# Kernel tuning notes

Hardware: AMD Instinct MI355X
Metric: run time of the kernel (lower is better)

The kernel has to match this reference:

```python
import jax, jax.numpy as jnp
import numpy as np

EMBED_DIM = 1024
NUM_HEADS = 16
HEAD_DIM = EMBED_DIM // NUM_HEADS


def setup_inputs() -> dict:
    key = jax.random.key(0)
    ks = jax.random.split(key, 6)
    B, S, D = 4, 2048, EMBED_DIM
    std = 1.0 / np.sqrt(D)
    x = jax.random.normal(ks[0], (B, S, D), dtype=jnp.float32)
    wq = jax.random.normal(ks[1], (D, D), dtype=jnp.float32) * std
    wk = jax.random.normal(ks[2], (D, D), dtype=jnp.float32) * std
    wv = jax.random.normal(ks[3], (D, D), dtype=jnp.float32) * std
    wo = jax.random.normal(ks[4], (D, D), dtype=jnp.float32) * std
    bo = jax.random.normal(ks[5], (D,), dtype=jnp.float32) * 0.01
    return {"x": x, "wq": wq, "wk": wk, "wv": wv, "wo": wo, "bo": bo}


def reference(x, wq, wk, wv, wo, bo):
    B, S, D = x.shape
    H, Hd = NUM_HEADS, HEAD_DIM
    scale = 1.0 / jnp.sqrt(jnp.asarray(Hd, x.dtype))
    # nn.Linear computes x @ W.T; split into heads -> [B, H, S, Hd]
    q = (x @ wq.T).reshape(B, S, H, Hd).transpose(0, 2, 1, 3)
    k = (x @ wk.T).reshape(B, S, H, Hd).transpose(0, 2, 1, 3)
    v = (x @ wv.T).reshape(B, S, H, Hd).transpose(0, 2, 1, 3)
    scores = jnp.einsum("bhqd,bhkd->bhqk", q, k) * scale  # [B,H,S,S]
    attn = jax.nn.softmax(scores, axis=-1)
    ctx = jnp.einsum("bhqk,bhkd->bhqd", attn, v)
    ctx = ctx.transpose(0, 2, 1, 3).reshape(B, S, D)
    return ctx @ wo.T + bo
```

## Files before the change

### kernel.cpp

```cpp
#include <hip/hip_runtime.h>

typedef __bf16 bf16x8 __attribute__((ext_vector_type(8)));
typedef float f32x4 __attribute__((ext_vector_type(4)));
typedef unsigned u32x4 __attribute__((ext_vector_type(4)));
typedef unsigned short u16;

#define GAS __attribute__((address_space(1)))
#define LAS __attribute__((address_space(3)))

static __device__ __forceinline__ void gload16(const void* g, void* l) {
  __builtin_amdgcn_global_load_lds((const GAS unsigned int*)g, (LAS unsigned int*)l, 16, 0, 0);
}

static __device__ __forceinline__ u16 f2bf(float f) {
  unsigned u = __builtin_bit_cast(unsigned, f);
  u += 0x7fffu + ((u >> 16) & 1u);
  return (u16)(u >> 16);
}

static __device__ __forceinline__ unsigned pk2(float lo, float hi) {
  ushort2 u;
  u.x = __builtin_bit_cast(u16, (__bf16)lo);
  u.y = __builtin_bit_cast(u16, (__bf16)hi);
  return __builtin_bit_cast(unsigned, u);
}

__global__ void cvt_all(const float* __restrict__ x, const float* __restrict__ wq,
                        const float* __restrict__ wk, const float* __restrict__ wv,
                        const float* __restrict__ wo, u16* __restrict__ xb,
                        u16* __restrict__ wqkvb, u16* __restrict__ wob) {
  int i = blockIdx.x * 256 + threadIdx.x;
  float4 v;
  ushort4* dst;
  if (i < 2097152) {
    v = reinterpret_cast<const float4*>(x)[i];
    dst = reinterpret_cast<ushort4*>(xb) + i;
  } else if (i < 2883584) {
    int j = i - 2097152;
    const float* s = j < 262144 ? wq : (j < 524288 ? wk : wv);
    int jj = j < 262144 ? j : (j < 524288 ? j - 262144 : j - 524288);
    v = reinterpret_cast<const float4*>(s)[jj];
    dst = reinterpret_cast<ushort4*>(wqkvb) + j;
  } else {
    int j = i - 2883584;
    v = reinterpret_cast<const float4*>(wo)[j];
    dst = reinterpret_cast<ushort4*>(wob) + j;
  }
  ushort4 o;
  o.x = f2bf(v.x); o.y = f2bf(v.y); o.z = f2bf(v.z); o.w = f2bf(v.w);
  *dst = o;
}

__global__ void gemm_qkv(const u16* __restrict__ A, const u16* __restrict__ W,
                         u16* __restrict__ Qo, u16* __restrict__ Ko, u16* __restrict__ Vo) {
  __shared__ u16 As[2 * 128 * 32];
  __shared__ u16 Bs[2 * 128 * 32];
  const int t = threadIdx.x;
  const int lane = t & 63;
  const int w = t >> 6;
  const int wr = w >> 1, wc = w & 1;
  const int l15 = lane & 15, lhi = lane >> 4;
  const int swz = (blockIdx.x & 7) * 192 + (blockIdx.x >> 3);
  const int bm = swz / 24, bn = swz % 24;

  f32x4 acc[4][4];
#pragma unroll
  for (int a = 0; a < 4; ++a)
#pragma unroll
    for (int b = 0; b < 4; ++b) acc[a][b] = (f32x4){0.f, 0.f, 0.f, 0.f};

  const u16* ag = A + (size_t)(bm * 128 + (t >> 2)) * 1024 + (t & 3) * 8;
  const u16* bg = W + (size_t)(bn * 128 + (t >> 2)) * 1024 + (t & 3) * 8;

  auto stage = [&](int cb, int kt) {
    gload16(ag + kt * 32, &As[cb + t * 8]);
    gload16(ag + kt * 32 + 64 * 1024, &As[cb + t * 8 + 2048]);
    gload16(bg + kt * 32, &Bs[cb + t * 8]);
    gload16(bg + kt * 32 + 64 * 1024, &Bs[cb + t * 8 + 2048]);
  };

  stage(0, 0);
  asm volatile("s_waitcnt vmcnt(0)" ::: "memory");
  __builtin_amdgcn_s_barrier();

  for (int kt = 0; kt < 32; ++kt) {
    const int cb = (kt & 1) * 4096;
    if (kt < 31) stage(cb ^ 4096, kt + 1);
    bf16x8 af[4], bfr[4];
#pragma unroll
    for (int mt = 0; mt < 4; ++mt)
      af[mt] = *(const bf16x8*)&As[cb + (wr * 64 + mt * 16 + l15) * 32 + lhi * 8];
#pragma unroll
    for (int nt = 0; nt < 4; ++nt)
      bfr[nt] = *(const bf16x8*)&Bs[cb + (wc * 64 + nt * 16 + l15) * 32 + lhi * 8];
#pragma unroll
    for (int mt = 0; mt < 4; ++mt)
#pragma unroll
      for (int nt = 0; nt < 4; ++nt)
        acc[mt][nt] = __builtin_amdgcn_mfma_f32_16x16x32_bf16(af[mt], bfr[nt], acc[mt][nt], 0, 0, 0);
    asm volatile("s_waitcnt vmcnt(0)" ::: "memory");
    __builtin_amdgcn_s_barrier();
  }

  const int tsel = bn >> 3;
  const int m0 = bm * 128 + wr * 64;
  const int n0 = bn * 128 + wc * 64;
  const int bb = bm >> 4;
  if (tsel == 0) {
    const float qs = 0.125f * 1.4426950408889634f;
#pragma unroll
    for (int nt = 0; nt < 4; ++nt) {
      int n = n0 + nt * 16 + l15;
      int c = n & 1023, h = c >> 6, hd = c & 63;
      size_t base = (size_t)(bb * 16 + h) * 2048 * 64 + hd;
#pragma unroll
      for (int mt = 0; mt < 4; ++mt)
#pragma unroll
        for (int i = 0; i < 4; ++i) {
          int s = (m0 + mt * 16 + lhi * 4 + i) & 2047;
          Qo[base + (size_t)s * 64] = f2bf(acc[mt][nt][i] * qs);
        }
    }
  } else if (tsel == 1) {
#pragma unroll
    for (int nt = 0; nt < 4; ++nt) {
      int n = n0 + nt * 16 + l15;
      int c = n & 1023, h = c >> 6, hd = c & 63;
      size_t base = (size_t)(bb * 16 + h) * 2048 * 64 + hd;
#pragma unroll
      for (int mt = 0; mt < 4; ++mt)
#pragma unroll
        for (int i = 0; i < 4; ++i) {
          int s = (m0 + mt * 16 + lhi * 4 + i) & 2047;
          Ko[base + (size_t)s * 64] = f2bf(acc[mt][nt][i]);
        }
    }
  } else {
#pragma unroll
    for (int nt = 0; nt < 4; ++nt) {
      int n = n0 + nt * 16 + l15;
      int c = n & 1023, h = c >> 6, hd = c & 63;
#pragma unroll
      for (int mt = 0; mt < 4; ++mt) {
        int s0 = (m0 + mt * 16 + lhi * 4) & 2047;
        int sp0 = ((s0 >> 4) & 1) * 4 + ((s0 >> 2) & 3) * 8 + (s0 >> 5) * 32;
        ushort4 pk;
        pk.x = f2bf(acc[mt][nt][0]);
        pk.y = f2bf(acc[mt][nt][1]);
        pk.z = f2bf(acc[mt][nt][2]);
        pk.w = f2bf(acc[mt][nt][3]);
        *(ushort4*)&Vo[((size_t)(bb * 16 + h) * 64 + hd) * 2048 + sp0] = pk;
      }
    }
  }
}

__global__ __launch_bounds__(256, 4) void attn_kernel(const u16* __restrict__ Q,
                                                      const u16* __restrict__ K,
                                                      const u16* __restrict__ Vp,
                                                      u16* __restrict__ Ctx) {
  __shared__ u16 Ks[2 * 64 * 64];
  __shared__ u16 Vs[2 * 64 * 64];
  const int t = threadIdx.x;
  const int lane = t & 63;
  const int w = t >> 6;
  const int l15 = lane & 15, lhi = lane >> 4;
  const int swz = (blockIdx.x & 7) * 128 + (blockIdx.x >> 3);
  const int qt = swz & 15, pair = swz >> 4;
  const u16* qp = Q + (size_t)pair * 2048 * 64;
  const u16* kp = K + (size_t)pair * 2048 * 64;
  const u16* vp = Vp + (size_t)pair * 64 * 2048;

  const int qrA = qt * 128 + w * 32 + l15;
  bf16x8 qfA[2], qfB[2];
  qfA[0] = *(const bf16x8*)&qp[(size_t)qrA * 64 + lhi * 8];
  qfA[1] = *(const bf16x8*)&qp[(size_t)qrA * 64 + 32 + lhi * 8];
  qfB[0] = *(const bf16x8*)&qp[(size_t)(qrA + 16) * 64 + lhi * 8];
  qfB[1] = *(const bf16x8*)&qp[(size_t)(qrA + 16) * 64 + 32 + lhi * 8];

  const u32x4 ow = {0x3F803F80u, 0x3F803F80u, 0x3F803F80u, 0x3F803F80u};
  const bf16x8 onesf = __builtin_bit_cast(bf16x8, ow);

  const int swzq = (l15 & 7) << 3;
  const int kofs0 = l15 * 64 + ((lhi * 8) ^ swzq);
  const int kofs1 = l15 * 64 + ((32 + lhi * 8) ^ swzq);
  const int vofs0 = l15 * 64 + ((lhi * 8) ^ swzq);
  const int vofs1 = l15 * 64 + ((32 + lhi * 8) ^ swzq);

  f32x4 coA[4], coB[4], laA, laB;
  laA = (f32x4){0.f, 0.f, 0.f, 0.f};
  laB = laA;
#pragma unroll
  for (int n = 0; n < 4; ++n) { coA[n] = laA; coB[n] = laA; }

  auto stage = [&](int cb, int tt) {
#pragma unroll
    for (int j = 0; j < 2; ++j) {
      int c = j * 256 + t;
      int r = c >> 3, c8 = (c & 7) * 8;
      gload16(kp + (size_t)(tt * 64 + r) * 64 + (c8 ^ ((r & 7) << 3)), &Ks[cb + c * 8]);
    }
#pragma unroll
    for (int j = 0; j < 2; ++j) {
      int c = j * 256 + t;
      int r = c >> 3, c8 = (c & 7) * 8;
      gload16(vp + (size_t)r * 2048 + tt * 64 + (c8 ^ ((r & 7) << 3)), &Vs[cb + c * 8]);
    }
  };

  auto softmax_sub = [&](f32x4 (&sa)[4], unsigned (&pw)[4][2]) {
#pragma unroll
    for (int nt = 0; nt < 4; ++nt)
#pragma unroll
      for (int e = 0; e < 4; ++e) sa[nt][e] = __builtin_exp2f(sa[nt][e]);
#pragma unroll
    for (int nt = 0; nt < 4; ++nt) {
      pw[nt][0] = pk2(sa[nt][0], sa[nt][1]);
      pw[nt][1] = pk2(sa[nt][2], sa[nt][3]);
    }
  };

  stage(0, 0);
  asm volatile("s_waitcnt vmcnt(0)" ::: "memory");
  __builtin_amdgcn_s_barrier();

  for (int kt = 0; kt < 32; ++kt) {
    const int cb = (kt & 1) * 4096;
    if (kt < 31) stage(cb ^ 4096, kt + 1);

    f32x4 saA[4], saB[4];
    __builtin_amdgcn_s_setprio(1);
#pragma unroll
    for (int nt = 0; nt < 4; ++nt) {
      bf16x8 kf0 = *(const bf16x8*)&Ks[cb + kofs0 + nt * 1024];
      bf16x8 kf1 = *(const bf16x8*)&Ks[cb + kofs1 + nt * 1024];
      f32x4 zA = (f32x4){0.f, 0.f, 0.f, 0.f};
      f32x4 zB = zA;
      zA = __builtin_amdgcn_mfma_f32_16x16x32_bf16(kf0, qfA[0], zA, 0, 0, 0);
      zB = __builtin_amdgcn_mfma_f32_16x16x32_bf16(kf0, qfB[0], zB, 0, 0, 0);
      saA[nt] = __builtin_amdgcn_mfma_f32_16x16x32_bf16(kf1, qfA[1], zA, 0, 0, 0);
      saB[nt] = __builtin_amdgcn_mfma_f32_16x16x32_bf16(kf1, qfB[1], zB, 0, 0, 0);
    }
    __builtin_amdgcn_s_setprio(0);

    unsigned pwA[4][2], pwB[4][2];
    softmax_sub(saA, pwA);
    softmax_sub(saB, pwB);

    __builtin_amdgcn_s_setprio(1);
#pragma unroll
    for (int ks = 0; ks < 2; ++ks) {
      u32x4 awA = {pwA[2 * ks][0], pwA[2 * ks][1], pwA[2 * ks + 1][0], pwA[2 * ks + 1][1]};
      u32x4 awB = {pwB[2 * ks][0], pwB[2 * ks][1], pwB[2 * ks + 1][0], pwB[2 * ks + 1][1]};
      bf16x8 afA = __builtin_bit_cast(bf16x8, awA);
      bf16x8 afB = __builtin_bit_cast(bf16x8, awB);
      laA = __builtin_amdgcn_mfma_f32_16x16x32_bf16(afA, onesf, laA, 0, 0, 0);
      laB = __builtin_amdgcn_mfma_f32_16x16x32_bf16(afB, onesf, laB, 0, 0, 0);
      const int vo = ks ? vofs1 : vofs0;
#pragma unroll
      for (int nthd = 0; nthd < 4; ++nthd) {
        bf16x8 vf = *(const bf16x8*)&Vs[cb + vo + nthd * 1024];
        coA[nthd] = __builtin_amdgcn_mfma_f32_16x16x32_bf16(afA, vf, coA[nthd], 0, 0, 0);
        coB[nthd] = __builtin_amdgcn_mfma_f32_16x16x32_bf16(afB, vf, coB[nthd], 0, 0, 0);
      }
    }
    __builtin_amdgcn_s_setprio(0);

    asm volatile("s_waitcnt vmcnt(0)" ::: "memory");
    __builtin_amdgcn_s_barrier();
  }

  float liA[4], liB[4];
#pragma unroll
  for (int i = 0; i < 4; ++i) {
    liA[i] = 1.0f / laA[i];
    liB[i] = 1.0f / laB[i];
  }
  const int bb = pair >> 4, hh = pair & 15;
  const int sbase = qt * 128 + w * 32 + lhi * 4;
#pragma unroll
  for (int nthd = 0; nthd < 4; ++nthd) {
    int hd = nthd * 16 + l15;
#pragma unroll
    for (int i = 0; i < 4; ++i) {
      Ctx[(size_t)(bb * 2048 + sbase + i) * 1024 + hh * 64 + hd] = f2bf(coA[nthd][i] * liA[i]);
      Ctx[(size_t)(bb * 2048 + sbase + 16 + i) * 1024 + hh * 64 + hd] = f2bf(coB[nthd][i] * liB[i]);
    }
  }
}

__global__ void gemm_out(const u16* __restrict__ A, const u16* __restrict__ W,
                         const float* __restrict__ Bo, float* __restrict__ Out) {
  __shared__ u16 As[2 * 128 * 32];
  __shared__ u16 Bs[2 * 128 * 32];
  const int t = threadIdx.x;
  const int lane = t & 63;
  const int w = t >> 6;
  const int wr = w >> 1, wc = w & 1;
  const int l15 = lane & 15, lhi = lane >> 4;
  const int swz = (blockIdx.x & 7) * 64 + (blockIdx.x >> 3);
  const int bm = swz >> 3, bn = swz & 7;

  f32x4 acc[4][4];
#pragma unroll
  for (int a = 0; a < 4; ++a)
#pragma unroll
    for (int b = 0; b < 4; ++b) acc[a][b] = (f32x4){0.f, 0.f, 0.f, 0.f};

  const u16* ag = A + (size_t)(bm * 128 + (t >> 2)) * 1024 + (t & 3) * 8;
  const u16* bg = W + (size_t)(bn * 128 + (t >> 2)) * 1024 + (t & 3) * 8;

  auto stage = [&](int cb, int kt) {
    gload16(ag + kt * 32, &As[cb + t * 8]);
    gload16(ag + kt * 32 + 64 * 1024, &As[cb + t * 8 + 2048]);
    gload16(bg + kt * 32, &Bs[cb + t * 8]);
    gload16(bg + kt * 32 + 64 * 1024, &Bs[cb + t * 8 + 2048]);
  };

  stage(0, 0);
  asm volatile("s_waitcnt vmcnt(0)" ::: "memory");
  __builtin_amdgcn_s_barrier();

  for (int kt = 0; kt < 32; ++kt) {
    const int cb = (kt & 1) * 4096;
    if (kt < 31) stage(cb ^ 4096, kt + 1);
    bf16x8 af[4], bfr[4];
#pragma unroll
    for (int mt = 0; mt < 4; ++mt)
      af[mt] = *(const bf16x8*)&As[cb + (wr * 64 + mt * 16 + l15) * 32 + lhi * 8];
#pragma unroll
    for (int nt = 0; nt < 4; ++nt)
      bfr[nt] = *(const bf16x8*)&Bs[cb + (wc * 64 + nt * 16 + l15) * 32 + lhi * 8];
#pragma unroll
    for (int mt = 0; mt < 4; ++mt)
#pragma unroll
      for (int nt = 0; nt < 4; ++nt)
        acc[mt][nt] = __builtin_amdgcn_mfma_f32_16x16x32_bf16(af[mt], bfr[nt], acc[mt][nt], 0, 0, 0);
    asm volatile("s_waitcnt vmcnt(0)" ::: "memory");
    __builtin_amdgcn_s_barrier();
  }

  const int m0 = bm * 128 + wr * 64;
  const int n0 = bn * 128 + wc * 64;
#pragma unroll
  for (int nt = 0; nt < 4; ++nt) {
    int n = n0 + nt * 16 + l15;
    float bias = Bo[n];
#pragma unroll
    for (int mt = 0; mt < 4; ++mt)
#pragma unroll
      for (int i = 0; i < 4; ++i) {
        int m = m0 + mt * 16 + lhi * 4 + i;
        Out[(size_t)m * 1024 + n] = acc[mt][nt][i] + bias;
      }
  }
}

extern "C" void kernel_launch(void* const* d_in, const int* in_sizes, int n_in,
                              void* d_out, int out_size, void* d_ws, size_t ws_size,
                              hipStream_t stream) {
  const float* x  = (const float*)d_in[0];
  const float* wq = (const float*)d_in[1];
  const float* wk = (const float*)d_in[2];
  const float* wv = (const float*)d_in[3];
  const float* wo = (const float*)d_in[4];
  const float* bo = (const float*)d_in[5];
  float* out = (float*)d_out;

  u16* xb    = (u16*)d_ws;
  u16* wqkvb = xb + (size_t)8 * 1024 * 1024;
  u16* wob   = wqkvb + (size_t)3 * 1024 * 1024;
  u16* qb    = wob + (size_t)1 * 1024 * 1024;
  u16* kb    = qb + (size_t)8 * 1024 * 1024;
  u16* vtb   = kb + (size_t)8 * 1024 * 1024;
  u16* ctxb  = xb;

  cvt_all<<<12288, 256, 0, stream>>>(x, wq, wk, wv, wo, xb, wqkvb, wob);
  gemm_qkv<<<64 * 24, 256, 0, stream>>>(xb, wqkvb, qb, kb, vtb);
  attn_kernel<<<1024, 256, 0, stream>>>(qb, kb, vtb, ctxb);
  gemm_out<<<64 * 8, 256, 0, stream>>>(ctxb, wob, bo, out);
}
```

Before: 213.4 us.

## Switch attention kernel from 16x16x32 to 32x32x16 MFMA tiles

Rewrites the attention inner loop to use 32x32x16 bf16 MFMA instructions, with each wave handling 32 query rows as one tile instead of two 16-row tiles. The V layout permutation written by the projection kernel changes so the P fragments produced by the 32x32 accumulator line up with V in LDS. This cuts the MFMA instruction count and the LDS fragment reads per tile, raising the compute-to-load ratio. In exchange, the larger 16-wide accumulators raise register pressure and lengthen MFMA dependency chains.

```diff
diff --git a/kernel.cpp b/kernel.cpp
--- a/kernel.cpp
+++ b/kernel.cpp
@@ -2,6 +2,7 @@
 
 typedef __bf16 bf16x8 __attribute__((ext_vector_type(8)));
 typedef float f32x4 __attribute__((ext_vector_type(4)));
+typedef float f32x16 __attribute__((ext_vector_type(16)));
 typedef unsigned u32x4 __attribute__((ext_vector_type(4)));
 typedef unsigned short u16;
 
@@ -143,13 +144,13 @@
 #pragma unroll
       for (int mt = 0; mt < 4; ++mt) {
         int s0 = (m0 + mt * 16 + lhi * 4) & 2047;
-        int sp0 = ((s0 >> 4) & 1) * 4 + ((s0 >> 2) & 3) * 8 + (s0 >> 5) * 32;
+        int p0 = (s0 & ~12) | (((s0 >> 2) & 1) << 3) | (((s0 >> 3) & 1) << 2);
         ushort4 pk;
         pk.x = f2bf(acc[mt][nt][0]);
         pk.y = f2bf(acc[mt][nt][1]);
         pk.z = f2bf(acc[mt][nt][2]);
         pk.w = f2bf(acc[mt][nt][3]);
-        *(ushort4*)&Vo[((size_t)(bb * 16 + h) * 64 + hd) * 2048 + sp0] = pk;
+        *(ushort4*)&Vo[((size_t)(bb * 16 + h) * 64 + hd) * 2048 + p0] = pk;
       }
     }
   }
@@ -164,34 +165,30 @@
   const int t = threadIdx.x;
   const int lane = t & 63;
   const int w = t >> 6;
-  const int l15 = lane & 15, lhi = lane >> 4;
+  const int l31 = lane & 31, hi = lane >> 5;
   const int swz = (blockIdx.x & 7) * 128 + (blockIdx.x >> 3);
   const int qt = swz & 15, pair = swz >> 4;
   const u16* qp = Q + (size_t)pair * 2048 * 64;
   const u16* kp = K + (size_t)pair * 2048 * 64;
   const u16* vp = Vp + (size_t)pair * 64 * 2048;
 
-  const int qrA = qt * 128 + w * 32 + l15;
-  bf16x8 qfA[2], qfB[2];
-  qfA[0] = *(const bf16x8*)&qp[(size_t)qrA * 64 + lhi * 8];
-  qfA[1] = *(const bf16x8*)&qp[(size_t)qrA * 64 + 32 + lhi * 8];
-  qfB[0] = *(const bf16x8*)&qp[(size_t)(qrA + 16) * 64 + lhi * 8];
-  qfB[1] = *(const bf16x8*)&qp[(size_t)(qrA + 16) * 64 + 32 + lhi * 8];
+  const int qrow = qt * 128 + w * 32 + l31;
+  bf16x8 qf[4];
+#pragma unroll
+  for (int d = 0; d < 4; ++d)
+    qf[d] = *(const bf16x8*)&qp[(size_t)qrow * 64 + d * 16 + hi * 8];
 
   const u32x4 ow = {0x3F803F80u, 0x3F803F80u, 0x3F803F80u, 0x3F803F80u};
   const bf16x8 onesf = __builtin_bit_cast(bf16x8, ow);
 
-  const int swzq = (l15 & 7) << 3;
-  const int kofs0 = l15 * 64 + ((lhi * 8) ^ swzq);
-  const int kofs1 = l15 * 64 + ((32 + lhi * 8) ^ swzq);
-  const int vofs0 = l15 * 64 + ((lhi * 8) ^ swzq);
-  const int vofs1 = l15 * 64 + ((32 + lhi * 8) ^ swzq);
-
-  f32x4 coA[4], coB[4], laA, laB;
-  laA = (f32x4){0.f, 0.f, 0.f, 0.f};
-  laB = laA;
-#pragma unroll
-  for (int n = 0; n < 4; ++n) { coA[n] = laA; coB[n] = laA; }
+  const int swzk = (l31 & 7) << 3;
+  int kc[4];
+#pragma unroll
+  for (int d = 0; d < 4; ++d) kc[d] = (d * 16 + hi * 8) ^ swzk;
+
+  const f32x16 fz = {0.f, 0.f, 0.f, 0.f, 0.f, 0.f, 0.f, 0.f,
+                     0.f, 0.f, 0.f, 0.f, 0.f, 0.f, 0.f, 0.f};
+  f32x16 co0 = fz, co1 = fz, la = fz;
 
   auto stage = [&](int cb, int tt) {
 #pragma unroll
@@ -208,18 +205,6 @@
     }
   };
 
-  auto softmax_sub = [&](f32x4 (&sa)[4], unsigned (&pw)[4][2]) {
-#pragma unroll
-    for (int nt = 0; nt < 4; ++nt)
-#pragma unroll
-      for (int e = 0; e < 4; ++e) sa[nt][e] = __builtin_exp2f(sa[nt][e]);
-#pragma unroll
-    for (int nt = 0; nt < 4; ++nt) {
-      pw[nt][0] = pk2(sa[nt][0], sa[nt][1]);
-      pw[nt][1] = pk2(sa[nt][2], sa[nt][3]);
-    }
-  };
-
   stage(0, 0);
   asm volatile("s_waitcnt vmcnt(0)" ::: "memory");
   __builtin_amdgcn_s_barrier();
@@ -228,64 +213,58 @@
     const int cb = (kt & 1) * 4096;
     if (kt < 31) stage(cb ^ 4096, kt + 1);
 
-    f32x4 saA[4], saB[4];
-    __builtin_amdgcn_s_setprio(1);
-#pragma unroll
-    for (int nt = 0; nt < 4; ++nt) {
-      bf16x8 kf0 = *(const bf16x8*)&Ks[cb + kofs0 + nt * 1024];
-      bf16x8 kf1 = *(const bf16x8*)&Ks[cb + kofs1 + nt * 1024];
-      f32x4 zA = (f32x4){0.f, 0.f, 0.f, 0.f};
-      f32x4 zB = zA;
-      zA = __builtin_amdgcn_mfma_f32_16x16x32_bf16(kf0, qfA[0], zA, 0, 0, 0);
-      zB = __builtin_amdgcn_mfma_f32_16x16x32_bf16(kf0, qfB[0], zB, 0, 0, 0);
-      saA[nt] = __builtin_amdgcn_mfma_f32_16x16x32_bf16(kf1, qfA[1], zA, 0, 0, 0);
-      saB[nt] = __builtin_amdgcn_mfma_f32_16x16x32_bf16(kf1, qfB[1], zB, 0, 0, 0);
-    }
-    __builtin_amdgcn_s_setprio(0);
-
-    unsigned pwA[4][2], pwB[4][2];
-    softmax_sub(saA, pwA);
-    softmax_sub(saB, pwB);
-
-    __builtin_amdgcn_s_setprio(1);
-#pragma unroll
-    for (int ks = 0; ks < 2; ++ks) {
-      u32x4 awA = {pwA[2 * ks][0], pwA[2 * ks][1], pwA[2 * ks + 1][0], pwA[2 * ks + 1][1]};
-      u32x4 awB = {pwB[2 * ks][0], pwB[2 * ks][1], pwB[2 * ks + 1][0], pwB[2 * ks + 1][1]};
-      bf16x8 afA = __builtin_bit_cast(bf16x8, awA);
-      bf16x8 afB = __builtin_bit_cast(bf16x8, awB);
-      laA = __builtin_amdgcn_mfma_f32_16x16x32_bf16(afA, onesf, laA, 0, 0, 0);
-      laB = __builtin_amdgcn_mfma_f32_16x16x32_bf16(afB, onesf, laB, 0, 0, 0);
-      const int vo = ks ? vofs1 : vofs0;
-#pragma unroll
-      for (int nthd = 0; nthd < 4; ++nthd) {
-        bf16x8 vf = *(const bf16x8*)&Vs[cb + vo + nthd * 1024];
-        coA[nthd] = __builtin_amdgcn_mfma_f32_16x16x32_bf16(afA, vf, coA[nthd], 0, 0, 0);
-        coB[nthd] = __builtin_amdgcn_mfma_f32_16x16x32_bf16(afB, vf, coB[nthd], 0, 0, 0);
+#pragma unroll
+    for (int ph = 0; ph < 2; ++ph) {
+      const int krow = cb + ph * 2048 + l31 * 64;
+      f32x16 sa;
+      __builtin_amdgcn_s_setprio(1);
+      {
+        bf16x8 kf0 = *(const bf16x8*)&Ks[krow + kc[0]];
+        bf16x8 kf1 = *(const bf16x8*)&Ks[krow + kc[1]];
+        bf16x8 kf2 = *(const bf16x8*)&Ks[krow + kc[2]];
+        bf16x8 kf3 = *(const bf16x8*)&Ks[krow + kc[3]];
+        sa = __builtin_amdgcn_mfma_f32_32x32x16_bf16(kf0, qf[0], fz, 0, 0, 0);
+        sa = __builtin_amdgcn_mfma_f32_32x32x16_bf16(kf1, qf[1], sa, 0, 0, 0);
+        sa = __builtin_amdgcn_mfma_f32_32x32x16_bf16(kf2, qf[2], sa, 0, 0, 0);
+        sa = __builtin_amdgcn_mfma_f32_32x32x16_bf16(kf3, qf[3], sa, 0, 0, 0);
       }
-    }
-    __builtin_amdgcn_s_setprio(0);
+      __builtin_amdgcn_s_setprio(0);
+
+#pragma unroll
+      for (int e = 0; e < 16; ++e) sa[e] = __builtin_exp2f(sa[e]);
+      unsigned pw[8];
+#pragma unroll
+      for (int r = 0; r < 8; ++r) pw[r] = pk2(sa[2 * r], sa[2 * r + 1]);
+
+      __builtin_amdgcn_s_setprio(1);
+#pragma unroll
+      for (int ss = 0; ss < 2; ++ss) {
+        u32x4 aw = {pw[4 * ss + 0], pw[4 * ss + 1], pw[4 * ss + 2], pw[4 * ss + 3]};
+        bf16x8 af = __builtin_bit_cast(bf16x8, aw);
+        la = __builtin_amdgcn_mfma_f32_32x32x16_bf16(af, onesf, la, 0, 0, 0);
+        const int s = ph * 2 + ss;
+        const int vcol = (s * 16 + hi * 8) ^ swzk;
+        bf16x8 vf0 = *(const bf16x8*)&Vs[cb + l31 * 64 + vcol];
+        bf16x8 vf1 = *(const bf16x8*)&Vs[cb + (32 + l31) * 64 + vcol];
+        co0 = __builtin_amdgcn_mfma_f32_32x32x16_bf16(af, vf0, co0, 0, 0, 0);
+        co1 = __builtin_amdgcn_mfma_f32_32x32x16_bf16(af, vf1, co1, 0, 0, 0);
+      }
+      __builtin_amdgcn_s_setprio(0);
+    }
 
     asm volatile("s_waitcnt vmcnt(0)" ::: "memory");
     __builtin_amdgcn_s_barrier();
   }
 
-  float liA[4], liB[4];
-#pragma unroll
-  for (int i = 0; i < 4; ++i) {
-    liA[i] = 1.0f / laA[i];
-    liB[i] = 1.0f / laB[i];
-  }
   const int bb = pair >> 4, hh = pair & 15;
-  const int sbase = qt * 128 + w * 32 + lhi * 4;
-#pragma unroll
-  for (int nthd = 0; nthd < 4; ++nthd) {
-    int hd = nthd * 16 + l15;
-#pragma unroll
-    for (int i = 0; i < 4; ++i) {
-      Ctx[(size_t)(bb * 2048 + sbase + i) * 1024 + hh * 64 + hd] = f2bf(coA[nthd][i] * liA[i]);
-      Ctx[(size_t)(bb * 2048 + sbase + 16 + i) * 1024 + hh * 64 + hd] = f2bf(coB[nthd][i] * liB[i]);
-    }
+  const int qbase = qt * 128 + w * 32 + 4 * hi;
+#pragma unroll
+  for (int r = 0; r < 16; ++r) {
+    int q = qbase + (r & 3) + 8 * (r >> 2);
+    float li = 1.0f / la[r];
+    size_t rowb = (size_t)(bb * 2048 + q) * 1024 + hh * 64;
+    Ctx[rowb + l31] = f2bf(co0[r] * li);
+    Ctx[rowb + 32 + l31] = f2bf(co1[r] * li);
   }
 }
 
```

Result: slower. 223.0 us (+4.5%).
